# Kernel tuning notes

Hardware: AMD Instinct MI355X
Metric: run time of the kernel (lower is better)

Reference implementation:

```python
import jax, jax.numpy as jnp
import numpy as np

N_WINDOW = 5
FEATS = 512
N_HIDDEN = 16
N = N_WINDOW * FEATS  # 2560


def leaky(x, slope):
    return jnp.where(x >= 0, x, slope * x)


def setup_inputs() -> dict:
    key = jax.random.key(0)
    ks = jax.random.split(key, 16)
    s = 0.05
    return {
        "data": jax.random.normal(ks[0], (1, N_WINDOW, FEATS), jnp.float32),
        "W1": jax.random.normal(ks[1], (N_HIDDEN, N), jnp.float32) * s,
        "b1": jax.random.normal(ks[2], (N_HIDDEN,), jnp.float32) * s,
        "W2": jax.random.normal(ks[3], (N_HIDDEN, N_HIDDEN), jnp.float32) * s,
        "b2": jax.random.normal(ks[4], (N_HIDDEN,), jnp.float32) * s,
        "W3": jax.random.normal(ks[5], (N_WINDOW, N_HIDDEN), jnp.float32) * s,
        "b3": jax.random.normal(ks[6], (N_WINDOW,), jnp.float32) * s,
        "gat_w": jax.random.normal(ks[7], (FEATS,), jnp.float32) * s,
        "a_src": jax.random.normal(ks[8], (FEATS,), jnp.float32) * s,
        "a_dst": jax.random.normal(ks[9], (FEATS,), jnp.float32) * s,
        "gat_bias": jax.random.normal(ks[10], (FEATS,), jnp.float32) * s,
        "F1": jax.random.normal(ks[11], (N_HIDDEN, FEATS), jnp.float32) * s,
        "fb1": jax.random.normal(ks[12], (N_HIDDEN,), jnp.float32) * s,
        "F2": jax.random.normal(ks[13], (N_WINDOW, N_HIDDEN), jnp.float32) * s,
        "fb2": jax.random.normal(ks[14], (N_WINDOW,), jnp.float32) * s,
    }


def reference(data, W1, b1, W2, b2, W3, b3, gat_w, a_src, a_dst, gat_bias, F1, fb1, F2, fb2):
    # ---- attention MLP: Flatten -> Linear -> LeakyReLU(1.0) -> Linear -> LeakyReLU(1.0) -> Linear -> Softmax(dim=0)
    flat = data.reshape(data.shape[0], -1)          # (1, n)
    h = leaky(flat @ W1.T + b1, 1.0)                 # slope True==1.0 -> identity (faithful)
    h = leaky(h @ W2.T + b2, 1.0)
    scores = h @ W3.T + b3                           # (1, n_window)
    att = jax.nn.softmax(scores, axis=0)             # softmax over batch dim (size 1 -> ones)
    att = att.reshape(-1, N_WINDOW, 1)               # (1, 5, 1)

    # ---- weighted window reduction: data_r = data^T @ att
    d = data.reshape(-1, N_WINDOW, FEATS)            # (1, 5, feats)
    data_r = jnp.matmul(jnp.swapaxes(d, -1, -2), att)  # (1, feats, 1)
    x = data_r.reshape(FEATS)                        # node features, scalar per node

    # ---- GATConv(in=1, out=1, heads=feats) on complete graph (self loops included)
    xW = x[:, None] * gat_w[None, :]                 # (N, H): per-head linear transform
    e_src = xW * a_src[None, :]                      # (N, H)
    e_dst = xW * a_dst[None, :]                      # (N, H)
    # logits e[i, j, h] for dst i, src j, head h
    e = leaky(e_dst[:, None, :] + e_src[None, :, :], 0.2)   # (N, N, H)
    alpha = jax.nn.softmax(e, axis=1)                # softmax over source nodes j
    feat_r = jnp.einsum('ijh,jh->ih', alpha, xW) + gat_bias  # (feats, feats)

    # ---- fcn: Linear -> LeakyReLU(1.0) -> Linear -> Sigmoid
    y = leaky(feat_r @ F1.T + fb1, 1.0)
    y = jax.nn.sigmoid(y @ F2.T + fb2)               # (feats, 5)
    return y.reshape(-1)
```

## Files before the change

### kernel.cpp

```cpp
#include <hip/hip_runtime.h>
#include <hip/hip_bf16.h>

#define FEATS 512
#define NW 5
#define NH 16
#define NOUT 5

#define GOFF 512
#define COFF (GOFF + NOUT * FEATS)
#define WS_FLOATS_NEEDED (COFF + NOUT)

template <int CTRL, int RMASK>
__device__ __forceinline__ float dpp_addf(float v) {
    const int r = __builtin_amdgcn_update_dpp(0, __float_as_int(v), CTRL, RMASK, 0xf, true);
    return v + __int_as_float(r);
}
__device__ __forceinline__ float scan64(float v) {
    v = dpp_addf<0x111, 0xf>(v);
    v = dpp_addf<0x112, 0xf>(v);
    v = dpp_addf<0x114, 0xf>(v);
    v = dpp_addf<0x118, 0xf>(v);
    v = dpp_addf<0x142, 0xa>(v);
    v = dpp_addf<0x143, 0xc>(v);
    return v;
}
template <int CTRL, int RMASK>
__device__ __forceinline__ int dpp_addi(int v) {
    const int r = __builtin_amdgcn_update_dpp(0, v, CTRL, RMASK, 0xf, true);
    return v + r;
}
__device__ __forceinline__ int scan64i(int v) {
    v = dpp_addi<0x111, 0xf>(v);
    v = dpp_addi<0x112, 0xf>(v);
    v = dpp_addi<0x114, 0xf>(v);
    v = dpp_addi<0x118, 0xf>(v);
    v = dpp_addi<0x142, 0xa>(v);
    v = dpp_addi<0x143, 0xc>(v);
    return v;
}

__global__ __launch_bounds__(512) void prep_sort(const float* __restrict__ data,
                                                 const float* __restrict__ F1,
                                                 const float* __restrict__ fb1,
                                                 const float* __restrict__ F2,
                                                 const float* __restrict__ fb2,
                                                 float* __restrict__ ws) {
    __shared__ float xs[FEATS];
    const int t = threadIdx.x;
    float v = 0.f;
    #pragma unroll
    for (int w = 0; w < NW; ++w) v += data[w * FEATS + t];
    xs[t] = v;
    __syncthreads();

    const int wid = t >> 6, lane = t & 63;
    const int i = blockIdx.x * 8 + wid;
    const float vi = xs[i];
    int r = 0;
    #pragma unroll
    for (int u = 0; u < 8; ++u) {
        const int j = u * 64 + lane;
        const float xj = xs[j];
        r += (xj < vi) || (xj == vi && j < i);
    }
    r = scan64i(r);
    if (lane == 63) ws[r] = vi;

    if (t < NOUT * 8) {
        const int o = t >> 3, hh = t & 7;
        const int h = blockIdx.x * 8 + hh;
        float g = 0.f;
        #pragma unroll
        for (int k = 0; k < NH; ++k) g = fmaf(F2[o * NH + k], F1[k * FEATS + h], g);
        ws[GOFF + o * FEATS + h] = g;
    }
    if (blockIdx.x == 0 && t < NOUT) {
        float c = fb2[t];
        #pragma unroll
        for (int k = 0; k < NH; ++k) c = fmaf(F2[t * NH + k], fb1[k], c);
        ws[COFF + t] = c;
    }
}

__global__ __launch_bounds__(512) void gat_all(
    const float* __restrict__ ws, const float* __restrict__ data,
    const float* __restrict__ gat_w, const float* __restrict__ a_src,
    const float* __restrict__ a_dst, const float* __restrict__ gat_bias,
    float* __restrict__ out)
{
    __shared__ float xsrt[FEATS];
    __shared__ float Mt[6 * 513];
    __shared__ float wt[6][8];
    __shared__ float part[NOUT][8];

    const int t = threadIdx.x, lane = t & 63, wid = t >> 6;
    const int i = blockIdx.x;
    const float LOG2E = 1.4426950408889634f;

    const float u = ws[t];
    xsrt[t] = u;

    const float u2 = u * u,  u3 = u2 * u, u4 = u3 * u, u5 = u4 * u, u6 = u5 * u;
    float s1 = scan64(u),  s2 = scan64(u2), s3 = scan64(u3);
    float s4 = scan64(u4), s5 = scan64(u5), s6 = scan64(u6);
    if (lane == 63) {
        wt[0][wid] = s1; wt[1][wid] = s2; wt[2][wid] = s3;
        wt[3][wid] = s4; wt[4][wid] = s5; wt[5][wid] = s6;
    }

    const float gw   = gat_w[t];
    const float asr  = a_src[t];
    const float ads  = a_dst[t];
    const float bias = gat_bias[t];
    float Gv[NOUT];
    #pragma unroll
    for (int o = 0; o < NOUT; ++o) Gv[o] = ws[GOFF + o * FEATS + t];
    float xi = 0.f;
    #pragma unroll
    for (int w = 0; w < NW; ++w) xi += data[w * FEATS + i];
    const float pv255 = ws[255], pv127 = ws[127], pv383 = ws[383];
    const float pv63  = ws[63],  pv191 = ws[191], pv319 = ws[319], pv447 = ws[447];

    __syncthreads();
    float o1 = 0, o2 = 0, o3 = 0, o4 = 0, o5 = 0, o6 = 0;
    #pragma unroll
    for (int w = 0; w < 7; ++w) {
        if (w < wid) {
            o1 += wt[0][w]; o2 += wt[1][w]; o3 += wt[2][w];
            o4 += wt[3][w]; o5 += wt[4][w]; o6 += wt[5][w];
        }
    }
    Mt[0 * 513 + t + 1] = s1 + o1;  Mt[1 * 513 + t + 1] = s2 + o2;
    Mt[2 * 513 + t + 1] = s3 + o3;  Mt[3 * 513 + t + 1] = s4 + o4;
    Mt[4 * 513 + t + 1] = s5 + o5;  Mt[5 * 513 + t + 1] = s6 + o6;
    if (t == 0) {
        #pragma unroll
        for (int p = 0; p < 6; ++p) Mt[p * 513] = 0.f;
    }
    __syncthreads();

    const float a  = gw * asr;
    const float d  = gw * ads * xi;
    const float a2 = 0.2f * a;
    const bool csn = (a >= 0.f);

    int m = 0;
    {
        float tt = fmaf(pv255, a, d);
        bool p = csn ? (tt >= 0.f) : (tt < 0.f);
        if (!p) m = 256;
        const float pvB = (m == 0) ? pv127 : pv383;
        tt = fmaf(pvB, a, d);
        p = csn ? (tt >= 0.f) : (tt < 0.f);
        if (!p) m += 128;
        const float pvC = (m & 256) ? ((m & 128) ? pv447 : pv319)
                                    : ((m & 128) ? pv191 : pv63);
        tt = fmaf(pvC, a, d);
        p = csn ? (tt >= 0.f) : (tt < 0.f);
        if (!p) m += 64;
    }
    #pragma unroll
    for (int step = 32; step; step >>= 1) {
        const int cand = m + step;
        const float tt = fmaf(xsrt[cand - 1], a, d);
        const bool p = csn ? (tt >= 0.f) : (tt < 0.f);
        if (!p) m = cand;
    }

    float P[6], N[6];
    #pragma unroll
    for (int p = 0; p < 6; ++p) {
        const float Pp = Mt[p * 513 + m];
        const float Tp = Mt[p * 513 + 512];
        P[p] = Pp; N[p] = Tp - Pp;
    }
    const float P0 = (float)m, N0 = (float)(FEATS - m);

    float Fv_[6], Qv_[6];
    #pragma unroll
    for (int p = 0; p < 6; ++p) { Fv_[p] = csn ? N[p] : P[p]; Qv_[p] = csn ? P[p] : N[p]; }
    const float F0 = csn ? N0 : P0;
    const float Q0 = csn ? P0 : N0;

    const float r2 = 0.5f, r3 = 1.f/6.f, r4 = 1.f/24.f, r5 = 1.f/120.f;
    float h;
    h = Fv_[4] * r5; h = fmaf(h, a, Fv_[3] * r4); h = fmaf(h, a, Fv_[2] * r3);
    h = fmaf(h, a, Fv_[1] * r2); h = fmaf(h, a, Fv_[0]);
    const float Fe = fmaf(h, a, F0);
    h = Fv_[5] * r5; h = fmaf(h, a, Fv_[4] * r4); h = fmaf(h, a, Fv_[3] * r3);
    h = fmaf(h, a, Fv_[2] * r2); h = fmaf(h, a, Fv_[1]);
    const float Fw = fmaf(h, a, Fv_[0]);
    h = Qv_[4] * r5; h = fmaf(h, a2, Qv_[3] * r4); h = fmaf(h, a2, Qv_[2] * r3);
    h = fmaf(h, a2, Qv_[1] * r2); h = fmaf(h, a2, Qv_[0]);
    const float Pe = fmaf(h, a2, Q0);
    h = Qv_[5] * r5; h = fmaf(h, a2, Qv_[4] * r4); h = fmaf(h, a2, Qv_[3] * r3);
    h = fmaf(h, a2, Qv_[2] * r2); h = fmaf(h, a2, Qv_[1]);
    const float Pw = fmaf(h, a2, Qv_[0]);

    const float A1 = __builtin_amdgcn_exp2f(LOG2E * d);
    const float A2 = __builtin_amdgcn_exp2f(0.2f * LOG2E * d);
    const float Se = A1 * Fe + A2 * Pe;
    const float Sv = A1 * Fw + A2 * Pw;
    const float feat = gw * (Sv / Se) + bias;

    #pragma unroll
    for (int o = 0; o < NOUT; ++o) {
        const float p = scan64(feat * Gv[o]);
        if (lane == 63) part[o][wid] = p;
    }
    __syncthreads();
    if (t < NOUT) {
        float s = ws[COFF + t];
        #pragma unroll
        for (int w = 0; w < 8; ++w) s += part[t][w];
        out[i * NOUT + t] = 1.f / (1.f + __builtin_amdgcn_exp2f(-s * LOG2E));
    }
}

__global__ __launch_bounds__(512) void gat_fused_fb(
    const float* __restrict__ data,
    const float* __restrict__ gat_w, const float* __restrict__ a_src,
    const float* __restrict__ a_dst, const float* __restrict__ gat_bias,
    const float* __restrict__ F1, const float* __restrict__ fb1,
    const float* __restrict__ F2, const float* __restrict__ fb2,
    float* __restrict__ out)
{
    __shared__ __align__(16) float xs[FEATS];
    __shared__ float feat[FEATS];
    __shared__ float part[NH][8];
    __shared__ float hv[NH];
    const int h = threadIdx.x;
    const int i = blockIdx.x;
    float v = 0.f;
    #pragma unroll
    for (int w = 0; w < NW; ++w) v += data[w * FEATS + h];
    xs[h] = v;
    __syncthreads();
    const float LOG2E = 1.4426950408889634f;
    const float gwv = gat_w[h];
    const float cs = gwv * a_src[h] * LOG2E;
    const float cd = gwv * a_dst[h] * LOG2E;
    const float di = xs[i] * cd;
    float se = 0.f, sv = 0.f;
    const float4* x4 = (const float4*)xs;
    for (int j4 = 0; j4 < FEATS / 4; ++j4) {
        float4 q = x4[j4];
        #pragma unroll
        for (int uu = 0; uu < 4; ++uu) {
            float xj = (uu == 0) ? q.x : (uu == 1) ? q.y : (uu == 2) ? q.z : q.w;
            float tt = fmaf(xj, cs, di);
            float l  = fmaxf(tt, 0.2f * tt);
            float e  = __builtin_amdgcn_exp2f(l);
            se += e;
            sv = fmaf(e, xj, sv);
        }
    }
    feat[h] = gwv * sv / se + gat_bias[h];
    __syncthreads();
    const int lane = h & 63, wid = h >> 6;
    const float fv = feat[h];
    for (int k = 0; k < NH; ++k) {
        float p = fv * F1[k * FEATS + h];
        #pragma unroll
        for (int off = 32; off; off >>= 1) p += __shfl_xor(p, off);
        if (lane == 0) part[k][wid] = p;
    }
    __syncthreads();
    if (h < NH) {
        float s = fb1[h];
        #pragma unroll
        for (int w = 0; w < 8; ++w) s += part[h][w];
        hv[h] = s;
    }
    __syncthreads();
    if (h < 5) {
        float s = fb2[h];
        #pragma unroll
        for (int k = 0; k < NH; ++k) s = fmaf(hv[k], F2[h * NH + k], s);
        out[i * 5 + h] = 1.f / (1.f + __builtin_amdgcn_exp2f(-s * LOG2E));
    }
}

extern "C" void kernel_launch(void* const* d_in, const int* in_sizes, int n_in,
                              void* d_out, int out_size, void* d_ws, size_t ws_size,
                              hipStream_t stream) {
    (void)in_sizes; (void)n_in; (void)out_size;
    const float* data     = (const float*)d_in[0];
    const float* gat_w    = (const float*)d_in[7];
    const float* a_src    = (const float*)d_in[8];
    const float* a_dst    = (const float*)d_in[9];
    const float* gat_bias = (const float*)d_in[10];
    const float* F1       = (const float*)d_in[11];
    const float* fb1      = (const float*)d_in[12];
    const float* F2       = (const float*)d_in[13];
    const float* fb2      = (const float*)d_in[14];
    float* out = (float*)d_out;

    if (ws_size >= (size_t)WS_FLOATS_NEEDED * sizeof(float)) {
        float* ws = (float*)d_ws;
        prep_sort<<<64, FEATS, 0, stream>>>(data, F1, fb1, F2, fb2, ws);
        gat_all<<<FEATS, FEATS, 0, stream>>>(ws, data, gat_w, a_src, a_dst, gat_bias, out);
    } else {
        gat_fused_fb<<<FEATS, FEATS, 0, stream>>>(data, gat_w, a_src, a_dst, gat_bias,
                                                  F1, fb1, F2, fb2, out);
    }
}
```

Baseline: 14.50 us.

## Process two destination nodes per 1024-thread block and split prefix-scan powers

```diff
diff --git a/kernel.cpp b/kernel.cpp
--- a/kernel.cpp
+++ b/kernel.cpp
@@ -82,7 +82,7 @@
     }
 }
 
-__global__ __launch_bounds__(512) void gat_all(
+__global__ __launch_bounds__(1024) void gat_all(
     const float* __restrict__ ws, const float* __restrict__ data,
     const float* __restrict__ gat_w, const float* __restrict__ a_src,
     const float* __restrict__ a_dst, const float* __restrict__ gat_bias,
@@ -91,30 +91,38 @@
     __shared__ float xsrt[FEATS];
     __shared__ float Mt[6 * 513];
     __shared__ float wt[6][8];
-    __shared__ float part[NOUT][8];
-
-    const int t = threadIdx.x, lane = t & 63, wid = t >> 6;
-    const int i = blockIdx.x;
+    __shared__ float part[2][NOUT][8];
+
+    const int t = threadIdx.x;
+    const int th = t & 511;
+    const int half = t >> 9;
+    const int lane = t & 63;
+    const int wid8 = (t >> 6) & 7;
+    const int i = blockIdx.x * 2 + half;
     const float LOG2E = 1.4426950408889634f;
 
-    const float u = ws[t];
-    xsrt[t] = u;
-
-    const float u2 = u * u,  u3 = u2 * u, u4 = u3 * u, u5 = u4 * u, u6 = u5 * u;
-    float s1 = scan64(u),  s2 = scan64(u2), s3 = scan64(u3);
-    float s4 = scan64(u4), s5 = scan64(u5), s6 = scan64(u6);
+    const float u = ws[th];
+    if (half == 0) xsrt[th] = u;
+
+    const float uu = u * u;
+    float b0, b1, b2;
+    if (half == 0) { b0 = u;       b1 = uu;      b2 = uu * u; }
+    else           { const float u4 = uu * uu;
+                     b0 = u4;      b1 = u4 * u;  b2 = u4 * uu; }
+    float s0 = scan64(b0), s1 = scan64(b1), s2 = scan64(b2);
     if (lane == 63) {
-        wt[0][wid] = s1; wt[1][wid] = s2; wt[2][wid] = s3;
-        wt[3][wid] = s4; wt[4][wid] = s5; wt[5][wid] = s6;
-    }
-
-    const float gw   = gat_w[t];
-    const float asr  = a_src[t];
-    const float ads  = a_dst[t];
-    const float bias = gat_bias[t];
+        wt[half * 3 + 0][wid8] = s0;
+        wt[half * 3 + 1][wid8] = s1;
+        wt[half * 3 + 2][wid8] = s2;
+    }
+
+    const float gw   = gat_w[th];
+    const float asr  = a_src[th];
+    const float ads  = a_dst[th];
+    const float bias = gat_bias[th];
     float Gv[NOUT];
     #pragma unroll
-    for (int o = 0; o < NOUT; ++o) Gv[o] = ws[GOFF + o * FEATS + t];
+    for (int o = 0; o < NOUT; ++o) Gv[o] = ws[GOFF + o * FEATS + th];
     float xi = 0.f;
     #pragma unroll
     for (int w = 0; w < NW; ++w) xi += data[w * FEATS + i];
@@ -122,17 +130,18 @@
     const float pv63  = ws[63],  pv191 = ws[191], pv319 = ws[319], pv447 = ws[447];
 
     __syncthreads();
-    float o1 = 0, o2 = 0, o3 = 0, o4 = 0, o5 = 0, o6 = 0;
+    float o0 = 0.f, o1 = 0.f, o2 = 0.f;
     #pragma unroll
     for (int w = 0; w < 7; ++w) {
-        if (w < wid) {
-            o1 += wt[0][w]; o2 += wt[1][w]; o3 += wt[2][w];
-            o4 += wt[3][w]; o5 += wt[4][w]; o6 += wt[5][w];
+        if (w < wid8) {
+            o0 += wt[half * 3 + 0][w];
+            o1 += wt[half * 3 + 1][w];
+            o2 += wt[half * 3 + 2][w];
         }
     }
-    Mt[0 * 513 + t + 1] = s1 + o1;  Mt[1 * 513 + t + 1] = s2 + o2;
-    Mt[2 * 513 + t + 1] = s3 + o3;  Mt[3 * 513 + t + 1] = s4 + o4;
-    Mt[4 * 513 + t + 1] = s5 + o5;  Mt[5 * 513 + t + 1] = s6 + o6;
+    Mt[(half * 3 + 0) * 513 + th + 1] = s0 + o0;
+    Mt[(half * 3 + 1) * 513 + th + 1] = s1 + o1;
+    Mt[(half * 3 + 2) * 513 + th + 1] = s2 + o2;
     if (t == 0) {
         #pragma unroll
         for (int p = 0; p < 6; ++p) Mt[p * 513] = 0.f;
@@ -206,14 +215,14 @@
     #pragma unroll
     for (int o = 0; o < NOUT; ++o) {
         const float p = scan64(feat * Gv[o]);
-        if (lane == 63) part[o][wid] = p;
-    }
-    __syncthreads();
-    if (t < NOUT) {
-        float s = ws[COFF + t];
-        #pragma unroll
-        for (int w = 0; w < 8; ++w) s += part[t][w];
-        out[i * NOUT + t] = 1.f / (1.f + __builtin_amdgcn_exp2f(-s * LOG2E));
+        if (lane == 63) part[half][o][wid8] = p;
+    }
+    __syncthreads();
+    if (th < NOUT) {
+        float s = ws[COFF + th];
+        #pragma unroll
+        for (int w = 0; w < 8; ++w) s += part[half][th][w];
+        out[i * NOUT + th] = 1.f / (1.f + __builtin_amdgcn_exp2f(-s * LOG2E));
     }
 }
 
@@ -299,7 +308,8 @@
     if (ws_size >= (size_t)WS_FLOATS_NEEDED * sizeof(float)) {
         float* ws = (float*)d_ws;
         prep_sort<<<64, FEATS, 0, stream>>>(data, F1, fb1, F2, fb2, ws);
-        gat_all<<<FEATS, FEATS, 0, stream>>>(ws, data, gat_w, a_src, a_dst, gat_bias, out);
+        gat_all<<<FEATS / 2, 1024, 0, stream>>>(ws, data, gat_w, a_src, a_dst,
+                                                gat_bias, out);
     } else {
         gat_fused_fb<<<FEATS, FEATS, 0, stream>>>(data, gat_w, a_src, a_dst, gat_bias,
                                                   F1, fb1, F2, fb2, out);
```

Result: no change. 14.57 us (+0.5%).
